# Performance work log

Measured on AMD Instinct MI355X. Metric: run time of the kernel, lower is better.

The kernel has to match this reference:

```python
import jax, jax.numpy as jnp
import numpy as np

B, K, T, V, H = 32, 5, 20, 9488, 1024


def setup_inputs() -> dict:
    key = jax.random.key(0)
    k0, k1, k2, k3, k4 = jax.random.split(key, 5)
    logprobs = jax.nn.log_softmax(jax.random.normal(k0, (B * K, V), jnp.float32), -1)
    beam_seq = jax.random.randint(k1, (B, K, T), 0, V)
    beam_seq_logprobs = jax.random.normal(k2, (B, K, T, V), jnp.float32)
    beam_logprobs_sum = jax.random.normal(k3, (B, K), jnp.float32)
    state = jax.random.normal(k4, (2, B * K, H), jnp.float32)
    return {"logprobs": logprobs, "beam_seq": beam_seq,
            "beam_seq_logprobs": beam_seq_logprobs,
            "beam_logprobs_sum": beam_logprobs_sum, "state": state,
            "beam_size": K, "t": T}


def reference(logprobs, beam_seq, beam_seq_logprobs, beam_logprobs_sum, state, beam_size, t):
    # One beam_step of CaptionModel.beam_search.
    batch = beam_logprobs_sum.shape[0]
    vocab = logprobs.shape[-1]
    lp = logprobs.reshape(batch, -1, vocab)                  # [B, K, V]
    cand = beam_logprobs_sum[:, :, None] + lp                # [B, K, V]
    flat = cand.reshape(batch, -1)                           # [B, K*V]
    # torch.sort(desc)[:, :beam_size] == top_k (sorted descending)
    ys, ix = jax.lax.top_k(flat, beam_size)                  # [B, K]
    beam_ix = ix // vocab                                    # source beam  [B, K]
    selected_ix = ix % vocab                                 # chosen word  [B, K]
    brange = jnp.arange(batch)[:, None]
    state_ix = (beam_ix + brange * lp.shape[1]).reshape(-1)  # [B*K]

    if t > 0:
        beam_seq = beam_seq[brange, beam_ix]                             # [B, K, t]
        beam_seq_logprobs = beam_seq_logprobs[brange, beam_ix]           # [B, K, t, V]
    beam_seq = jnp.concatenate([beam_seq, selected_ix[:, :, None].astype(beam_seq.dtype)], -1)

    beam_logprobs_sum = (jnp.take_along_axis(beam_logprobs_sum, beam_ix, 1)
                         + jnp.take_along_axis(lp.reshape(batch, -1), ix, 1))  # [B, K]

    beam_lp = lp[brange, beam_ix]                            # [B, K, V]
    beam_seq_logprobs = jnp.concatenate([beam_seq_logprobs, beam_lp[:, :, None, :]], 2)

    new_state = state[:, state_ix]                           # [layers, B*K, H]
    return beam_seq, beam_seq_logprobs, beam_logprobs_sum, new_state
```

## Files before the change

### kernel.cpp

```cpp
#include <hip/hip_runtime.h>

#define BB 32
#define KK 5
#define TT 20
#define VV 9488
#define HH 1024

#define NSPLIT 16
#define CHUNK (VV / NSPLIT)

#define OFF1 3360
#define OFF2 31883040
#define OFF3 31883200

__device__ __forceinline__ bool better(float av, int ai, float bv, int bi) {
    return (av > bv) || (av == bv && ai < bi);
}

__global__ __launch_bounds__(256) void topk_part_kernel(
    const float* __restrict__ logprobs,
    const float* __restrict__ sums,
    float* __restrict__ pv,
    int*   __restrict__ pi)
{
    const int b    = blockIdx.x / NSPLIT;
    const int part = blockIdx.x % NSPLIT;
    const int tid  = threadIdx.x;
    const int v0   = part * CHUNK;

    float tv[5]; int ti[5];
#pragma unroll
    for (int j = 0; j < 5; ++j) { tv[j] = -INFINITY; ti[j] = 0x7fffffff; }

    for (int k = 0; k < KK; ++k) {
        const float s = sums[b * KK + k];
        const float* lp = logprobs + (size_t)(b * KK + k) * VV;
        for (int v = v0 + tid; v < v0 + CHUNK; v += 256) {
            const float val = s + lp[v];
            const int idx = k * VV + v;
            if (better(val, idx, tv[4], ti[4])) {
                int pos = 4;
#pragma unroll
                for (int j = 3; j >= 0; --j)
                    if (better(val, idx, tv[j], ti[j])) pos = j;
#pragma unroll
                for (int j = 4; j > 0; --j) {
                    if (j > pos) { tv[j] = tv[j-1]; ti[j] = ti[j-1]; }
                }
                tv[pos] = val; ti[pos] = idx;
            }
        }
    }

    __shared__ float sv[256 * 5];
    __shared__ int   si[256 * 5];

    for (int stride = 128; stride >= 1; stride >>= 1) {
        if (tid >= stride && tid < 2 * stride) {
#pragma unroll
            for (int j = 0; j < 5; ++j) { sv[tid*5+j] = tv[j]; si[tid*5+j] = ti[j]; }
        }
        __syncthreads();
        if (tid < stride) {
            float bv[5]; int bi[5];
#pragma unroll
            for (int j = 0; j < 5; ++j) { bv[j] = sv[(tid+stride)*5+j]; bi[j] = si[(tid+stride)*5+j]; }
            float ov[5]; int oi[5];
            int ia = 0, ib = 0;
#pragma unroll
            for (int n = 0; n < 5; ++n) {
                if (better(tv[ia], ti[ia], bv[ib], bi[ib])) { ov[n] = tv[ia]; oi[n] = ti[ia]; ++ia; }
                else                                        { ov[n] = bv[ib]; oi[n] = bi[ib]; ++ib; }
            }
#pragma unroll
            for (int j = 0; j < 5; ++j) { tv[j] = ov[j]; ti[j] = oi[j]; }
        }
        __syncthreads();
    }

    if (tid == 0) {
#pragma unroll
        for (int j = 0; j < 5; ++j) {
            pv[(size_t)blockIdx.x * 5 + j] = tv[j];
            pi[(size_t)blockIdx.x * 5 + j] = ti[j];
        }
    }
}

__global__ __launch_bounds__(64) void topk_merge_kernel(
    const float* __restrict__ pv,
    const int*   __restrict__ pi,
    int* __restrict__ ws_beam,
    int* __restrict__ ws_sel,
    float* __restrict__ ws_sum)
{
    const int b   = blockIdx.x;
    const int tid = threadIdx.x;

    float tv[5]; int ti[5];
    if (tid < NSPLIT) {
#pragma unroll
        for (int j = 0; j < 5; ++j) {
            tv[j] = pv[((size_t)b * NSPLIT + tid) * 5 + j];
            ti[j] = pi[((size_t)b * NSPLIT + tid) * 5 + j];
        }
    } else {
#pragma unroll
        for (int j = 0; j < 5; ++j) { tv[j] = -INFINITY; ti[j] = 0x7fffffff; }
    }

    __shared__ float sv[NSPLIT * 5];
    __shared__ int   si[NSPLIT * 5];

    for (int stride = NSPLIT / 2; stride >= 1; stride >>= 1) {
        if (tid >= stride && tid < 2 * stride) {
#pragma unroll
            for (int j = 0; j < 5; ++j) { sv[tid*5+j] = tv[j]; si[tid*5+j] = ti[j]; }
        }
        __syncthreads();
        if (tid < stride) {
            float bv[5]; int bi[5];
#pragma unroll
            for (int j = 0; j < 5; ++j) { bv[j] = sv[(tid+stride)*5+j]; bi[j] = si[(tid+stride)*5+j]; }
            float ov[5]; int oi[5];
            int ia = 0, ib = 0;
#pragma unroll
            for (int n = 0; n < 5; ++n) {
                if (better(tv[ia], ti[ia], bv[ib], bi[ib])) { ov[n] = tv[ia]; oi[n] = ti[ia]; ++ia; }
                else                                        { ov[n] = bv[ib]; oi[n] = bi[ib]; ++ib; }
            }
#pragma unroll
            for (int j = 0; j < 5; ++j) { tv[j] = ov[j]; ti[j] = oi[j]; }
        }
        __syncthreads();
    }

    if (tid == 0) {
#pragma unroll
        for (int j = 0; j < 5; ++j) {
            const int idx  = ti[j];
            const int beam = idx / VV;
            const int sel  = idx - beam * VV;
            ws_beam[b * KK + j] = beam;
            ws_sel [b * KK + j] = sel;
            ws_sum [b * KK + j] = tv[j];
        }
    }
}

__global__ __launch_bounds__(256) void scatter_kernel(
    const float* __restrict__ logprobs,
    const int*   __restrict__ beam_seq_in,
    const float* __restrict__ bslp_in,
    const float* __restrict__ state_in,
    const int*   __restrict__ ws_beam,
    const int*   __restrict__ ws_sel,
    const float* __restrict__ ws_sum,
    float* __restrict__ out)
{
    const int bid = blockIdx.x;
    const int tid = threadIdx.x;
    const int NROWS = BB * KK * (TT + 1);

    if (bid < NROWS) {
        const int b   = bid / (KK * (TT + 1));
        const int rem = bid % (KK * (TT + 1));
        const int k   = rem / (TT + 1);
        const int t   = rem % (TT + 1);
        const int beam = ws_beam[b * KK + k];
        const float* src;
        if (t < TT) src = bslp_in + ((size_t)((b * KK + beam) * TT + t)) * VV;
        else        src = logprobs + (size_t)(b * KK + beam) * VV;
        float* dst = out + OFF1 + (size_t)bid * VV;
        const float4* s4 = (const float4*)src;
        float4* d4 = (float4*)dst;
        for (int i = tid; i < VV / 4; i += 256) d4[i] = s4[i];
    } else if (bid < NROWS + 2 * BB * KK) {
        const int r = bid - NROWS;
        const int s = r / (BB * KK);
        const int i = r % (BB * KK);
        const int b = i / KK;
        const int beam = ws_beam[i];
        const float4* s4 = (const float4*)(state_in + ((size_t)s * (BB * KK) + b * KK + beam) * HH);
        float4* d4 = (float4*)(out + OFF3 + (size_t)r * HH);
        for (int j = tid; j < HH / 4; j += 256) d4[j] = s4[j];
    } else {
        for (int j = tid; j < NROWS; j += 256) {
            const int b   = j / (KK * (TT + 1));
            const int rem = j % (KK * (TT + 1));
            const int k   = rem / (TT + 1);
            const int t   = rem % (TT + 1);
            const int bk  = b * KK + k;
            int val;
            if (t < TT) val = beam_seq_in[(size_t)(b * KK + ws_beam[bk]) * TT + t];
            else        val = ws_sel[bk];
            out[j] = (float)val;
        }
        for (int j = tid; j < BB * KK; j += 256) out[OFF2 + j] = ws_sum[j];
    }
}

extern "C" void kernel_launch(void* const* d_in, const int* in_sizes, int n_in,
                              void* d_out, int out_size, void* d_ws, size_t ws_size,
                              hipStream_t stream) {
    const float* logprobs    = (const float*)d_in[0];
    const int*   beam_seq    = (const int*)  d_in[1];
    const float* bslp        = (const float*)d_in[2];
    const float* sums        = (const float*)d_in[3];
    const float* state       = (const float*)d_in[4];

    int*   ws_beam = (int*)d_ws;
    int*   ws_sel  = ws_beam + BB * KK;
    float* ws_sum  = (float*)(ws_sel + BB * KK);
    float* pv      = ws_sum + BB * KK;
    int*   pi      = (int*)(pv + BB * NSPLIT * 5);
    float* out     = (float*)d_out;

    topk_part_kernel<<<BB * NSPLIT, 256, 0, stream>>>(logprobs, sums, pv, pi);
    topk_merge_kernel<<<BB, 64, 0, stream>>>(pv, pi, ws_beam, ws_sel, ws_sum);

    const int nblocks = BB * KK * (TT + 1) + 2 * BB * KK + 1;
    scatter_kernel<<<nblocks, 256, 0, stream>>>(logprobs, beam_seq, bslp, state,
                                                ws_beam, ws_sel, ws_sum, out);
}
```

Before: 61.94 us.

## Fuse top-k merge into scatter kernel and use wave shuffles for reductions

Removes the separate top-k merge kernel. Each scatter block now redoes the 16-way partial merge itself with wave-level shuffle merges and derives its source beam in place. The partial top-k kernel replaces its shared-memory tree reduction with xor-shuffle merges plus a small cross-wave step, and inserts candidates with branchless selects. The copy stores become nontemporal. This saves one launch and several barrier-heavy reduction rounds, at the cost of redundant merge work in every scatter block.

```diff
diff --git a/kernel.cpp b/kernel.cpp
--- a/kernel.cpp
+++ b/kernel.cpp
@@ -5,7 +5,6 @@
 #define TT 20
 #define VV 9488
 #define HH 1024
-
 #define NSPLIT 16
 #define CHUNK (VV / NSPLIT)
 
@@ -13,8 +12,58 @@
 #define OFF2 31883040
 #define OFF3 31883200
 
+typedef float f4 __attribute__((ext_vector_type(4)));
+
 __device__ __forceinline__ bool better(float av, int ai, float bv, int bi) {
     return (av > bv) || (av == bv && ai < bi);
+}
+
+__device__ __forceinline__ void insert5(float tv[5], int ti[5], float val, int idx) {
+#pragma unroll
+    for (int j = 4; j >= 1; --j) {
+        bool bj  = better(val, idx, tv[j],   ti[j]);
+        bool bj1 = better(val, idx, tv[j-1], ti[j-1]);
+        float nv = bj ? (bj1 ? tv[j-1] : val) : tv[j];
+        int   ni = bj ? (bj1 ? ti[j-1] : idx) : ti[j];
+        tv[j] = nv; ti[j] = ni;
+    }
+    bool b0 = better(val, idx, tv[0], ti[0]);
+    ti[0] = b0 ? idx : ti[0];
+    tv[0] = b0 ? val : tv[0];
+}
+
+__device__ __forceinline__ void merge_sorted5(float av[5], int ai[5],
+                                              const float bv[5], const int bi[5]) {
+    float ov[5]; int oi[5];
+#pragma unroll
+    for (int n = 0; n < 5; ++n) {
+        float mv = 0.f; int mi = 0;
+#pragma unroll
+        for (int i = 0; i <= n; ++i) {
+            const int j = n - i;
+            float cv; int ci;
+            if (better(av[i], ai[i], bv[j], bi[j])) { cv = av[i]; ci = ai[i]; }
+            else                                    { cv = bv[j]; ci = bi[j]; }
+            if (i == 0 || better(mv, mi, cv, ci)) { mv = cv; mi = ci; }
+        }
+        ov[n] = mv; oi[n] = mi;
+    }
+#pragma unroll
+    for (int n = 0; n < 5; ++n) { av[n] = ov[n]; ai[n] = oi[n]; }
+}
+
+template<int MAXST>
+__device__ __forceinline__ void wave_merge(float tv[5], int ti[5]) {
+#pragma unroll
+    for (int st = 1; st <= MAXST; st <<= 1) {
+        float bv[5]; int bi[5];
+#pragma unroll
+        for (int j = 0; j < 5; ++j) {
+            bv[j] = __shfl_xor(tv[j], st);
+            bi[j] = __shfl_xor(ti[j], st);
+        }
+        merge_sorted5(tv, ti, bv, bi);
+    }
 }
 
 __global__ __launch_bounds__(256) void topk_part_kernel(
@@ -30,120 +79,41 @@
 
     float tv[5]; int ti[5];
 #pragma unroll
-    for (int j = 0; j < 5; ++j) { tv[j] = -INFINITY; ti[j] = 0x7fffffff; }
-
+    for (int j = 0; j < 5; ++j) { tv[j] = -INFINITY; ti[j] = 0x7FFFFF00 + j; }
+
+#pragma unroll
     for (int k = 0; k < KK; ++k) {
         const float s = sums[b * KK + k];
         const float* lp = logprobs + (size_t)(b * KK + k) * VV;
-        for (int v = v0 + tid; v < v0 + CHUNK; v += 256) {
-            const float val = s + lp[v];
-            const int idx = k * VV + v;
-            if (better(val, idx, tv[4], ti[4])) {
-                int pos = 4;
-#pragma unroll
-                for (int j = 3; j >= 0; --j)
-                    if (better(val, idx, tv[j], ti[j])) pos = j;
-#pragma unroll
-                for (int j = 4; j > 0; --j) {
-                    if (j > pos) { tv[j] = tv[j-1]; ti[j] = ti[j-1]; }
-                }
-                tv[pos] = val; ti[pos] = idx;
+        for (int v = v0 + tid; v < v0 + CHUNK; v += 256)
+            insert5(tv, ti, s + lp[v], k * VV + v);
+    }
+
+    wave_merge<32>(tv, ti);
+
+    __shared__ float lv[4][5];
+    __shared__ int   li[4][5];
+    const int wid = tid >> 6, lane = tid & 63;
+    if (lane == 0) {
+#pragma unroll
+        for (int j = 0; j < 5; ++j) { lv[wid][j] = tv[j]; li[wid][j] = ti[j]; }
+    }
+    __syncthreads();
+    if (tid < 64) {
+        if (tid < 4) {
+#pragma unroll
+            for (int j = 0; j < 5; ++j) { tv[j] = lv[tid][j]; ti[j] = li[tid][j]; }
+        } else {
+#pragma unroll
+            for (int j = 0; j < 5; ++j) { tv[j] = -INFINITY; ti[j] = 0x7FFFFF00 + j; }
+        }
+        wave_merge<2>(tv, ti);
+        if (tid == 0) {
+#pragma unroll
+            for (int j = 0; j < 5; ++j) {
+                pv[(size_t)blockIdx.x * 5 + j] = tv[j];
+                pi[(size_t)blockIdx.x * 5 + j] = ti[j];
             }
-        }
-    }
-
-    __shared__ float sv[256 * 5];
-    __shared__ int   si[256 * 5];
-
-    for (int stride = 128; stride >= 1; stride >>= 1) {
-        if (tid >= stride && tid < 2 * stride) {
-#pragma unroll
-            for (int j = 0; j < 5; ++j) { sv[tid*5+j] = tv[j]; si[tid*5+j] = ti[j]; }
-        }
-        __syncthreads();
-        if (tid < stride) {
-            float bv[5]; int bi[5];
-#pragma unroll
-            for (int j = 0; j < 5; ++j) { bv[j] = sv[(tid+stride)*5+j]; bi[j] = si[(tid+stride)*5+j]; }
-            float ov[5]; int oi[5];
-            int ia = 0, ib = 0;
-#pragma unroll
-            for (int n = 0; n < 5; ++n) {
-                if (better(tv[ia], ti[ia], bv[ib], bi[ib])) { ov[n] = tv[ia]; oi[n] = ti[ia]; ++ia; }
-                else                                        { ov[n] = bv[ib]; oi[n] = bi[ib]; ++ib; }
-            }
-#pragma unroll
-            for (int j = 0; j < 5; ++j) { tv[j] = ov[j]; ti[j] = oi[j]; }
-        }
-        __syncthreads();
-    }
-
-    if (tid == 0) {
-#pragma unroll
-        for (int j = 0; j < 5; ++j) {
-            pv[(size_t)blockIdx.x * 5 + j] = tv[j];
-            pi[(size_t)blockIdx.x * 5 + j] = ti[j];
-        }
-    }
-}
-
-__global__ __launch_bounds__(64) void topk_merge_kernel(
-    const float* __restrict__ pv,
-    const int*   __restrict__ pi,
-    int* __restrict__ ws_beam,
-    int* __restrict__ ws_sel,
-    float* __restrict__ ws_sum)
-{
-    const int b   = blockIdx.x;
-    const int tid = threadIdx.x;
-
-    float tv[5]; int ti[5];
-    if (tid < NSPLIT) {
-#pragma unroll
-        for (int j = 0; j < 5; ++j) {
-            tv[j] = pv[((size_t)b * NSPLIT + tid) * 5 + j];
-            ti[j] = pi[((size_t)b * NSPLIT + tid) * 5 + j];
-        }
-    } else {
-#pragma unroll
-        for (int j = 0; j < 5; ++j) { tv[j] = -INFINITY; ti[j] = 0x7fffffff; }
-    }
-
-    __shared__ float sv[NSPLIT * 5];
-    __shared__ int   si[NSPLIT * 5];
-
-    for (int stride = NSPLIT / 2; stride >= 1; stride >>= 1) {
-        if (tid >= stride && tid < 2 * stride) {
-#pragma unroll
-            for (int j = 0; j < 5; ++j) { sv[tid*5+j] = tv[j]; si[tid*5+j] = ti[j]; }
-        }
-        __syncthreads();
-        if (tid < stride) {
-            float bv[5]; int bi[5];
-#pragma unroll
-            for (int j = 0; j < 5; ++j) { bv[j] = sv[(tid+stride)*5+j]; bi[j] = si[(tid+stride)*5+j]; }
-            float ov[5]; int oi[5];
-            int ia = 0, ib = 0;
-#pragma unroll
-            for (int n = 0; n < 5; ++n) {
-                if (better(tv[ia], ti[ia], bv[ib], bi[ib])) { ov[n] = tv[ia]; oi[n] = ti[ia]; ++ia; }
-                else                                        { ov[n] = bv[ib]; oi[n] = bi[ib]; ++ib; }
-            }
-#pragma unroll
-            for (int j = 0; j < 5; ++j) { tv[j] = ov[j]; ti[j] = oi[j]; }
-        }
-        __syncthreads();
-    }
-
-    if (tid == 0) {
-#pragma unroll
-        for (int j = 0; j < 5; ++j) {
-            const int idx  = ti[j];
-            const int beam = idx / VV;
-            const int sel  = idx - beam * VV;
-            ws_beam[b * KK + j] = beam;
-            ws_sel [b * KK + j] = sel;
-            ws_sum [b * KK + j] = tv[j];
         }
     }
 }
@@ -153,73 +123,89 @@
     const int*   __restrict__ beam_seq_in,
     const float* __restrict__ bslp_in,
     const float* __restrict__ state_in,
-    const int*   __restrict__ ws_beam,
-    const int*   __restrict__ ws_sel,
-    const float* __restrict__ ws_sum,
+    const float* __restrict__ pv,
+    const int*   __restrict__ pi,
     float* __restrict__ out)
 {
-    const int bid = blockIdx.x;
-    const int tid = threadIdx.x;
-    const int NROWS = BB * KK * (TT + 1);
-
-    if (bid < NROWS) {
-        const int b   = bid / (KK * (TT + 1));
-        const int rem = bid % (KK * (TT + 1));
-        const int k   = rem / (TT + 1);
-        const int t   = rem % (TT + 1);
-        const int beam = ws_beam[b * KK + k];
-        const float* src;
-        if (t < TT) src = bslp_in + ((size_t)((b * KK + beam) * TT + t)) * VV;
-        else        src = logprobs + (size_t)(b * KK + beam) * VV;
-        float* dst = out + OFF1 + (size_t)bid * VV;
-        const float4* s4 = (const float4*)src;
-        float4* d4 = (float4*)dst;
-        for (int i = tid; i < VV / 4; i += 256) d4[i] = s4[i];
-    } else if (bid < NROWS + 2 * BB * KK) {
-        const int r = bid - NROWS;
-        const int s = r / (BB * KK);
-        const int i = r % (BB * KK);
-        const int b = i / KK;
-        const int beam = ws_beam[i];
-        const float4* s4 = (const float4*)(state_in + ((size_t)s * (BB * KK) + b * KK + beam) * HH);
-        float4* d4 = (float4*)(out + OFF3 + (size_t)r * HH);
-        for (int j = tid; j < HH / 4; j += 256) d4[j] = s4[j];
+    const int bid  = blockIdx.x;
+    const int tid  = threadIdx.x;
+    const int lane = tid & 63;
+
+    int b, k = 0, t = 0, role, r = 0;
+    if (bid < 3360)      { role = 0; b = bid / 105; int rem = bid % 105; k = rem / 21; t = rem % 21; }
+    else if (bid < 3680) { role = 1; r = bid - 3360; int i = r % 160; b = i / 5; k = i % 5; }
+    else                 { role = 2; b = bid - 3680; }
+
+    float tv[5]; int ti[5];
+    if (lane < NSPLIT) {
+        const size_t base = ((size_t)b * NSPLIT + lane) * 5;
+#pragma unroll
+        for (int j = 0; j < 5; ++j) { tv[j] = pv[base + j]; ti[j] = pi[base + j]; }
     } else {
-        for (int j = tid; j < NROWS; j += 256) {
-            const int b   = j / (KK * (TT + 1));
-            const int rem = j % (KK * (TT + 1));
-            const int k   = rem / (TT + 1);
-            const int t   = rem % (TT + 1);
-            const int bk  = b * KK + k;
-            int val;
-            if (t < TT) val = beam_seq_in[(size_t)(b * KK + ws_beam[bk]) * TT + t];
-            else        val = ws_sel[bk];
-            out[j] = (float)val;
-        }
-        for (int j = tid; j < BB * KK; j += 256) out[OFF2 + j] = ws_sum[j];
+#pragma unroll
+        for (int j = 0; j < 5; ++j) { tv[j] = -INFINITY; ti[j] = 0x7FFFFF00 + j; }
+    }
+    wave_merge<32>(tv, ti);
+
+    if (role == 0) {
+        int sidx = 0;
+#pragma unroll
+        for (int j = 0; j < 5; ++j) if (k == j) sidx = ti[j];
+        const int beam = sidx / VV;
+        const float* src = (t < TT)
+            ? bslp_in  + ((size_t)((b * KK + beam) * TT + t)) * VV
+            : logprobs + (size_t)(b * KK + beam) * VV;
+        const f4* s4 = (const f4*)src;
+        f4* d4 = (f4*)(out + OFF1 + (size_t)bid * VV);
+        for (int i = tid; i < VV / 4; i += 256) {
+            f4 v = s4[i];
+            __builtin_nontemporal_store(v, &d4[i]);
+        }
+    } else if (role == 1) {
+        const int s = r / 160;
+        int sidx = 0;
+#pragma unroll
+        for (int j = 0; j < 5; ++j) if (k == j) sidx = ti[j];
+        const int beam = sidx / VV;
+        const f4* s4 = (const f4*)(state_in + ((size_t)s * (BB * KK) + b * KK + beam) * HH);
+        f4* d4 = (f4*)(out + OFF3 + (size_t)r * HH);
+        for (int j = tid; j < HH / 4; j += 256) {
+            f4 v = s4[j];
+            __builtin_nontemporal_store(v, &d4[j]);
+        }
+    } else {
+        if (tid < 105) {
+            const int k2 = tid / 21, t2 = tid % 21;
+            int sidx = 0;
+#pragma unroll
+            for (int j = 0; j < 5; ++j) if (k2 == j) sidx = ti[j];
+            const int beam = sidx / VV;
+            const int sel  = sidx - beam * VV;
+            const int val  = (t2 < TT) ? beam_seq_in[(size_t)(b * KK + beam) * TT + t2] : sel;
+            out[(size_t)b * 105 + tid] = (float)val;
+        }
+#pragma unroll
+        for (int j = 0; j < 5; ++j)
+            if (tid == 105 + j) out[OFF2 + b * KK + j] = tv[j];
     }
 }
 
 extern "C" void kernel_launch(void* const* d_in, const int* in_sizes, int n_in,
                               void* d_out, int out_size, void* d_ws, size_t ws_size,
                               hipStream_t stream) {
-    const float* logprobs    = (const float*)d_in[0];
-    const int*   beam_seq    = (const int*)  d_in[1];
-    const float* bslp        = (const float*)d_in[2];
-    const float* sums        = (const float*)d_in[3];
-    const float* state       = (const float*)d_in[4];
-
-    int*   ws_beam = (int*)d_ws;
-    int*   ws_sel  = ws_beam + BB * KK;
-    float* ws_sum  = (float*)(ws_sel + BB * KK);
-    float* pv      = ws_sum + BB * KK;
-    int*   pi      = (int*)(pv + BB * NSPLIT * 5);
-    float* out     = (float*)d_out;
+    const float* logprobs = (const float*)d_in[0];
+    const int*   beam_seq = (const int*)  d_in[1];
+    const float* bslp     = (const float*)d_in[2];
+    const float* sums     = (const float*)d_in[3];
+    const float* state    = (const float*)d_in[4];
+
+    float* pv = (float*)d_ws;
+    int*   pi = (int*)(pv + BB * NSPLIT * 5);
+    float* out = (float*)d_out;
 
     topk_part_kernel<<<BB * NSPLIT, 256, 0, stream>>>(logprobs, sums, pv, pi);
-    topk_merge_kernel<<<BB, 64, 0, stream>>>(pv, pi, ws_beam, ws_sel, ws_sum);
-
-    const int nblocks = BB * KK * (TT + 1) + 2 * BB * KK + 1;
+
+    const int nblocks = 3360 + 320 + 32;
     scatter_kernel<<<nblocks, 256, 0, stream>>>(logprobs, beam_seq, bslp, state,
-                                                ws_beam, ws_sel, ws_sum, out);
-}
+                                                pv, pi, out);
+}
```

Measured after the change: 65.75 us. +6.2%, slower.
